# Kernel optimization log

Hardware: AMD Instinct MI355X
Metric: run time of the kernel (lower is better)

The kernel has to match this reference:

```python
import jax, jax.numpy as jnp
import numpy as np

HEADS = 4
DIM_HEAD = 128
SCALE = DIM_HEAD ** (-0.5)


def setup_inputs() -> dict:
    key = jax.random.key(0)
    k1, k2 = jax.random.split(key)
    fmap = jax.random.normal(k1, (1, 256, 64, 64), dtype=jnp.float32)
    # 1x1 conv weight, no bias: [out_channels=2*heads*dim_head, in_channels=dim]
    W_qk = jax.random.normal(k2, (1024, 256), dtype=jnp.float32) * (256 ** -0.5)
    return {"fmap": fmap, "W_qk": W_qk}


def reference(fmap, W_qk):
    b, c, h, w = fmap.shape
    # 1x1 conv == channel-wise matmul
    qk = jnp.einsum('bcxy,oc->boxy', fmap, W_qk)  # [b, 2*heads*dim_head, h, w]
    q, k = jnp.split(qk, 2, axis=1)
    def to_bhxyd(t):
        # 'b (h d) x y -> b h x y d'
        return t.reshape(b, HEADS, DIM_HEAD, h, w).transpose(0, 1, 3, 4, 2)
    q = to_bhxyd(q) * SCALE
    k = to_bhxyd(k)
    sim = jnp.einsum('bhxyd,bhuvd->bhxyuv', q, k)
    sim = sim.reshape(b, HEADS, h * w, h * w)
    return jax.nn.softmax(sim, axis=-1)
```

## Files before the change

### kernel.cpp

```cpp
#include <hip/hip_runtime.h>
#include <math.h>

#define HEADS 4
#define DHEAD 128
#define NPOS  4096
#define CIN   256
#define SCALEF 0.08838834764831845f
#define LOG2E  1.4426950408889634f
#define QSCALE (SCALEF * LOG2E)

typedef _Float16 half8  __attribute__((ext_vector_type(8)));
typedef _Float16 half4  __attribute__((ext_vector_type(4)));
typedef _Float16 half2v __attribute__((ext_vector_type(2)));
typedef float    f32x4  __attribute__((ext_vector_type(4)));

#define FRAG_HEAD_HALVES (256 * 4 * 512)

__global__ __launch_bounds__(256) void cvt_kernel(const float* __restrict__ fmap,
                                                  const float* __restrict__ W,
                                                  _Float16* __restrict__ W16,
                                                  _Float16* __restrict__ fmapT) {
  if (blockIdx.x < 16) {
    int base = blockIdx.x * 16384 + threadIdx.x;
#pragma unroll
    for (int t = 0; t < 64; ++t) {
      int idx = base + t * 256;
      float v = W[idx];
      W16[idx] = (_Float16)(idx < 512 * CIN ? v * QSCALE : v);
    }
  } else {
    int tile = blockIdx.x - 16;
    int p0 = (tile >> 2) * 64, c0 = (tile & 3) * 64;
    __shared__ float t_lds[64][65];
    int tid = threadIdx.x;
#pragma unroll
    for (int t = 0; t < 16; ++t) {
      int lin = tid + t * 256;
      int r = lin >> 6, col = lin & 63;
      t_lds[r][col] = fmap[(size_t)(c0 + r) * NPOS + p0 + col];
    }
    __syncthreads();
#pragma unroll
    for (int t = 0; t < 16; ++t) {
      int lin = tid + t * 256;
      int pr = lin >> 6, cc = lin & 63;
      fmapT[(size_t)(p0 + pr) * CIN + c0 + cc] = (_Float16)t_lds[cc][pr];
    }
  }
}

__global__ __launch_bounds__(256) void proj_mfma(const _Float16* __restrict__ W16,
                                                 const _Float16* __restrict__ fmapT,
                                                 _Float16* __restrict__ qf,
                                                 _Float16* __restrict__ kf) {
  const int p0 = blockIdx.x * 64;
  const int o0 = blockIdx.y * 64 + (threadIdx.x >> 6) * 16;
  const int l = threadIdx.x & 63;
  const int lr = l & 15, lg = l >> 4;

  const f32x4 z = {0.f, 0.f, 0.f, 0.f};
  f32x4 acc[4] = {z, z, z, z};
#pragma unroll
  for (int kb = 0; kb < 8; ++kb) {
    half8 a = *(const half8*)(W16 + (size_t)(o0 + lr) * CIN + kb * 32 + lg * 8);
#pragma unroll
    for (int j = 0; j < 4; ++j) {
      half8 b = *(const half8*)(fmapT + (size_t)(p0 + j * 16 + lr) * CIN + kb * 32 + lg * 8);
      acc[j] = __builtin_amdgcn_mfma_f32_16x16x32_f16(a, b, acc[j], 0, 0, 0);
    }
  }
  const int ob = o0 + lg * 4;
  const bool isq = ob < 512;
  const int oo = isq ? ob : ob - 512;
  const int h = oo >> 7, db = oo & 127;
  const int kb2 = db >> 5;
  const int flane = ((db >> 3) & 3) * 16 + lr;
  const int e0 = db & 7;
  _Float16* dst = (isq ? qf : kf) + (size_t)h * FRAG_HEAD_HALVES;
#pragma unroll
  for (int j = 0; j < 4; ++j) {
    int pt = (p0 >> 4) + j;
    half4 v = {(_Float16)acc[j][0], (_Float16)acc[j][1],
               (_Float16)acc[j][2], (_Float16)acc[j][3]};
    *(half4*)(dst + ((size_t)pt * 4 + kb2) * 512 + flane * 8 + e0) = v;
  }
}

#define QROWS 16
#define NTIL  32

__global__ __launch_bounds__(512) void attn_mfma(const _Float16* __restrict__ qf,
                                                 const _Float16* __restrict__ kf,
                                                 float* __restrict__ out) {
  const int h = blockIdx.y;
  const int i0 = blockIdx.x * QROWS;
  const int wv = threadIdx.x >> 6;
  const int l = threadIdx.x & 63;
  const int lr = l & 15, lg = l >> 4;

  const _Float16* Qf = qf + (size_t)h * FRAG_HEAD_HALVES;
  const _Float16* Kf = kf + (size_t)h * FRAG_HEAD_HALVES;

  half8 afr[4];
#pragma unroll
  for (int kb = 0; kb < 4; ++kb)
    afr[kb] = *(const half8*)(Qf + ((size_t)(i0 >> 4) * 4 + kb) * 512 + l * 8);

  const int jt0 = wv * NTIL;
  half2v Pst[2 * NTIL];
  float rs[4] = {0.f, 0.f, 0.f, 0.f};
  const f32x4 z = {0.f, 0.f, 0.f, 0.f};

#pragma unroll
  for (int t = 0; t < NTIL; ++t) {
    const _Float16* kp = Kf + ((size_t)(jt0 + t) * 4) * 512 + l * 8;
    half8 b0 = *(const half8*)(kp);
    half8 b1 = *(const half8*)(kp + 512);
    half8 b2 = *(const half8*)(kp + 1024);
    half8 b3 = *(const half8*)(kp + 1536);
    f32x4 acc = z;
    __builtin_amdgcn_s_setprio(1);
    acc = __builtin_amdgcn_mfma_f32_16x16x32_f16(afr[0], b0, acc, 0, 0, 0);
    acc = __builtin_amdgcn_mfma_f32_16x16x32_f16(afr[1], b1, acc, 0, 0, 0);
    acc = __builtin_amdgcn_mfma_f32_16x16x32_f16(afr[2], b2, acc, 0, 0, 0);
    acc = __builtin_amdgcn_mfma_f32_16x16x32_f16(afr[3], b3, acc, 0, 0, 0);
    __builtin_amdgcn_s_setprio(0);
    float e0 = __builtin_amdgcn_exp2f(acc[0]);
    float e1 = __builtin_amdgcn_exp2f(acc[1]);
    float e2 = __builtin_amdgcn_exp2f(acc[2]);
    float e3 = __builtin_amdgcn_exp2f(acc[3]);
    rs[0] += e0; rs[1] += e1; rs[2] += e2; rs[3] += e3;
    Pst[2 * t]     = half2v{(_Float16)e0, (_Float16)e1};
    Pst[2 * t + 1] = half2v{(_Float16)e2, (_Float16)e3};
  }

#pragma unroll
  for (int off = 1; off < 16; off <<= 1) {
#pragma unroll
    for (int r = 0; r < 4; ++r) rs[r] += __shfl_xor(rs[r], off);
  }
  __shared__ float red[8][16];
  if (lr == 0) {
#pragma unroll
    for (int r = 0; r < 4; ++r) red[wv][lg * 4 + r] = rs[r];
  }
  __syncthreads();
  float inv[4];
#pragma unroll
  for (int r = 0; r < 4; ++r) {
    float s = 0.f;
#pragma unroll
    for (int w = 0; w < 8; ++w) s += red[w][lg * 4 + r];
    inv[r] = 1.0f / s;
  }

  float* ob = out + ((size_t)h * NPOS + i0) * NPOS + jt0 * 16;
#pragma unroll
  for (int t = 0; t < NTIL; ++t) {
    float e[4] = {(float)Pst[2 * t][0], (float)Pst[2 * t][1],
                  (float)Pst[2 * t + 1][0], (float)Pst[2 * t + 1][1]};
#pragma unroll
    for (int r = 0; r < 4; ++r) {
      ob[(size_t)(lg * 4 + r) * NPOS + t * 16 + lr] = e[r] * inv[r];
    }
  }
}

extern "C" void kernel_launch(void* const* d_in, const int* in_sizes, int n_in,
                              void* d_out, int out_size, void* d_ws, size_t ws_size,
                              hipStream_t stream) {
  const float* fmap = (const float*)d_in[0];
  const float* W    = (const float*)d_in[1];
  float* out = (float*)d_out;

  char* ws = (char*)d_ws;
  _Float16* qf    = (_Float16*)(ws);
  _Float16* kf    = (_Float16*)(ws + (4u << 20));
  _Float16* W16   = (_Float16*)(ws + (8u << 20));
  _Float16* fmapT = (_Float16*)(ws + (8u << 20) + (512u << 10));

  cvt_kernel<<<272, 256, 0, stream>>>(fmap, W, W16, fmapT);
  proj_mfma<<<dim3(NPOS / 64, 1024 / 64), 256, 0, stream>>>(W16, fmapT, qf, kf);
  attn_mfma<<<dim3(NPOS / QROWS, HEADS), 512, 0, stream>>>(qf, kf, out);
}
```

Before: 110.2 us.

## Recompute QK scores in second pass and reuse K fragments across four query tiles

The attention kernel now processes 64 query rows per block with 16 waves. Each wave loads a K fragment once and applies it to four query row tiles. The stored fp16 exponentials are replaced by a second pass that reloads K and recomputes the MFMA scores and exp2 before writing normalized outputs. This cuts register use from the stored probabilities and reduces K reloads per query row, at the cost of doubling the MFMA and exp work and running larger 1024-thread blocks.

```diff
diff --git a/kernel.cpp b/kernel.cpp
--- a/kernel.cpp
+++ b/kernel.cpp
@@ -11,7 +11,6 @@
 
 typedef _Float16 half8  __attribute__((ext_vector_type(8)));
 typedef _Float16 half4  __attribute__((ext_vector_type(4)));
-typedef _Float16 half2v __attribute__((ext_vector_type(2)));
 typedef float    f32x4  __attribute__((ext_vector_type(4)));
 
 #define FRAG_HEAD_HALVES (256 * 4 * 512)
@@ -86,12 +85,13 @@
   }
 }
 
-#define QROWS 16
-#define NTIL  32
-
-__global__ __launch_bounds__(512) void attn_mfma(const _Float16* __restrict__ qf,
-                                                 const _Float16* __restrict__ kf,
-                                                 float* __restrict__ out) {
+#define QROWS 64
+#define RT    4
+#define NTIL  16
+
+__global__ __launch_bounds__(1024) void attn_mfma(const _Float16* __restrict__ qf,
+                                                  const _Float16* __restrict__ kf,
+                                                  float* __restrict__ out) {
   const int h = blockIdx.y;
   const int i0 = blockIdx.x * QROWS;
   const int wv = threadIdx.x >> 6;
@@ -101,67 +101,94 @@
   const _Float16* Qf = qf + (size_t)h * FRAG_HEAD_HALVES;
   const _Float16* Kf = kf + (size_t)h * FRAG_HEAD_HALVES;
 
-  half8 afr[4];
-#pragma unroll
-  for (int kb = 0; kb < 4; ++kb)
-    afr[kb] = *(const half8*)(Qf + ((size_t)(i0 >> 4) * 4 + kb) * 512 + l * 8);
+  half8 afr[RT][4];
+#pragma unroll
+  for (int rt = 0; rt < RT; ++rt)
+#pragma unroll
+    for (int kb = 0; kb < 4; ++kb)
+      afr[rt][kb] = *(const half8*)(Qf + (((size_t)(i0 >> 4) + rt) * 4 + kb) * 512 + l * 8);
 
   const int jt0 = wv * NTIL;
-  half2v Pst[2 * NTIL];
-  float rs[4] = {0.f, 0.f, 0.f, 0.f};
+  const _Float16* kbase = Kf + (size_t)jt0 * 2048 + l * 8;
+
+  float rs[RT][4];
+#pragma unroll
+  for (int rt = 0; rt < RT; ++rt)
+#pragma unroll
+    for (int r = 0; r < 4; ++r) rs[rt][r] = 0.f;
   const f32x4 z = {0.f, 0.f, 0.f, 0.f};
 
 #pragma unroll
   for (int t = 0; t < NTIL; ++t) {
-    const _Float16* kp = Kf + ((size_t)(jt0 + t) * 4) * 512 + l * 8;
+    const _Float16* kp = kbase + (size_t)t * 2048;
     half8 b0 = *(const half8*)(kp);
     half8 b1 = *(const half8*)(kp + 512);
     half8 b2 = *(const half8*)(kp + 1024);
     half8 b3 = *(const half8*)(kp + 1536);
-    f32x4 acc = z;
-    __builtin_amdgcn_s_setprio(1);
-    acc = __builtin_amdgcn_mfma_f32_16x16x32_f16(afr[0], b0, acc, 0, 0, 0);
-    acc = __builtin_amdgcn_mfma_f32_16x16x32_f16(afr[1], b1, acc, 0, 0, 0);
-    acc = __builtin_amdgcn_mfma_f32_16x16x32_f16(afr[2], b2, acc, 0, 0, 0);
-    acc = __builtin_amdgcn_mfma_f32_16x16x32_f16(afr[3], b3, acc, 0, 0, 0);
-    __builtin_amdgcn_s_setprio(0);
-    float e0 = __builtin_amdgcn_exp2f(acc[0]);
-    float e1 = __builtin_amdgcn_exp2f(acc[1]);
-    float e2 = __builtin_amdgcn_exp2f(acc[2]);
-    float e3 = __builtin_amdgcn_exp2f(acc[3]);
-    rs[0] += e0; rs[1] += e1; rs[2] += e2; rs[3] += e3;
-    Pst[2 * t]     = half2v{(_Float16)e0, (_Float16)e1};
-    Pst[2 * t + 1] = half2v{(_Float16)e2, (_Float16)e3};
+#pragma unroll
+    for (int rt = 0; rt < RT; ++rt) {
+      f32x4 acc = z;
+      __builtin_amdgcn_s_setprio(1);
+      acc = __builtin_amdgcn_mfma_f32_16x16x32_f16(afr[rt][0], b0, acc, 0, 0, 0);
+      acc = __builtin_amdgcn_mfma_f32_16x16x32_f16(afr[rt][1], b1, acc, 0, 0, 0);
+      acc = __builtin_amdgcn_mfma_f32_16x16x32_f16(afr[rt][2], b2, acc, 0, 0, 0);
+      acc = __builtin_amdgcn_mfma_f32_16x16x32_f16(afr[rt][3], b3, acc, 0, 0, 0);
+      __builtin_amdgcn_s_setprio(0);
+      rs[rt][0] += __builtin_amdgcn_exp2f(acc[0]);
+      rs[rt][1] += __builtin_amdgcn_exp2f(acc[1]);
+      rs[rt][2] += __builtin_amdgcn_exp2f(acc[2]);
+      rs[rt][3] += __builtin_amdgcn_exp2f(acc[3]);
+    }
   }
 
 #pragma unroll
   for (int off = 1; off < 16; off <<= 1) {
 #pragma unroll
-    for (int r = 0; r < 4; ++r) rs[r] += __shfl_xor(rs[r], off);
-  }
-  __shared__ float red[8][16];
+    for (int rt = 0; rt < RT; ++rt)
+#pragma unroll
+      for (int r = 0; r < 4; ++r) rs[rt][r] += __shfl_xor(rs[rt][r], off);
+  }
+  __shared__ float red[16][QROWS];
   if (lr == 0) {
 #pragma unroll
-    for (int r = 0; r < 4; ++r) red[wv][lg * 4 + r] = rs[r];
+    for (int rt = 0; rt < RT; ++rt)
+#pragma unroll
+      for (int r = 0; r < 4; ++r) red[wv][rt * 16 + lg * 4 + r] = rs[rt][r];
   }
   __syncthreads();
-  float inv[4];
-#pragma unroll
-  for (int r = 0; r < 4; ++r) {
-    float s = 0.f;
-#pragma unroll
-    for (int w = 0; w < 8; ++w) s += red[w][lg * 4 + r];
-    inv[r] = 1.0f / s;
-  }
+  float inv[RT][4];
+#pragma unroll
+  for (int rt = 0; rt < RT; ++rt)
+#pragma unroll
+    for (int r = 0; r < 4; ++r) {
+      float s = 0.f;
+#pragma unroll
+      for (int w = 0; w < 16; ++w) s += red[w][rt * 16 + lg * 4 + r];
+      inv[rt][r] = 1.0f / s;
+    }
 
   float* ob = out + ((size_t)h * NPOS + i0) * NPOS + jt0 * 16;
 #pragma unroll
   for (int t = 0; t < NTIL; ++t) {
-    float e[4] = {(float)Pst[2 * t][0], (float)Pst[2 * t][1],
-                  (float)Pst[2 * t + 1][0], (float)Pst[2 * t + 1][1]};
-#pragma unroll
-    for (int r = 0; r < 4; ++r) {
-      ob[(size_t)(lg * 4 + r) * NPOS + t * 16 + lr] = e[r] * inv[r];
+    const _Float16* kp = kbase + (size_t)t * 2048;
+    half8 b0 = *(const half8*)(kp);
+    half8 b1 = *(const half8*)(kp + 512);
+    half8 b2 = *(const half8*)(kp + 1024);
+    half8 b3 = *(const half8*)(kp + 1536);
+#pragma unroll
+    for (int rt = 0; rt < RT; ++rt) {
+      f32x4 acc = z;
+      __builtin_amdgcn_s_setprio(1);
+      acc = __builtin_amdgcn_mfma_f32_16x16x32_f16(afr[rt][0], b0, acc, 0, 0, 0);
+      acc = __builtin_amdgcn_mfma_f32_16x16x32_f16(afr[rt][1], b1, acc, 0, 0, 0);
+      acc = __builtin_amdgcn_mfma_f32_16x16x32_f16(afr[rt][2], b2, acc, 0, 0, 0);
+      acc = __builtin_amdgcn_mfma_f32_16x16x32_f16(afr[rt][3], b3, acc, 0, 0, 0);
+      __builtin_amdgcn_s_setprio(0);
+      float* obr = ob + (size_t)(rt * 16 + lg * 4) * NPOS + t * 16 + lr;
+      obr[0]            = __builtin_amdgcn_exp2f(acc[0]) * inv[rt][0];
+      obr[NPOS]         = __builtin_amdgcn_exp2f(acc[1]) * inv[rt][1];
+      obr[2 * (size_t)NPOS] = __builtin_amdgcn_exp2f(acc[2]) * inv[rt][2];
+      obr[3 * (size_t)NPOS] = __builtin_amdgcn_exp2f(acc[3]) * inv[rt][3];
     }
   }
 }
@@ -181,5 +208,5 @@
 
   cvt_kernel<<<272, 256, 0, stream>>>(fmap, W, W16, fmapT);
   proj_mfma<<<dim3(NPOS / 64, 1024 / 64), 256, 0, stream>>>(W16, fmapT, qf, kf);
-  attn_mfma<<<dim3(NPOS / QROWS, HEADS), 512, 0, stream>>>(qf, kf, out);
-}
+  attn_mfma<<<dim3(NPOS / QROWS, HEADS), 1024, 0, stream>>>(qf, kf, out);
+}
```

New measurement: 303.3 us. +175.3%, slower.
